# Kernel optimization log

Hardware: AMD Instinct MI355X
Metric: run time of the kernel (lower is better)

## Reference

```python
import jax, jax.numpy as jnp
import numpy as np

N = 50000      # nodes
E = 800000     # edges (before self loops)
IN = 128       # in_channels
H = 8          # heads
C = 32         # hidden_channels per head
HC = H * C     # 256, concat head dim
G = 256        # number of graphs
NEG_SLOPE = 0.2  # PyG GATConv default


def gat_conv(h_in, src, dst, W, att_s, att_d, bias):
    """PyG-style GATConv, concat heads. src/dst include self loops.
    h_in: [N, F_in]; W: [H*C, F_in]; att_s/att_d: [H, C]; bias: [H*C]."""
    h = (h_in @ W.T).reshape(N, H, C)                      # [N,H,C]
    a_s = jnp.sum(h * att_s, axis=-1)                      # [N,H]
    a_d = jnp.sum(h * att_d, axis=-1)                      # [N,H]
    e = jax.nn.leaky_relu(a_s[src] + a_d[dst], NEG_SLOPE)  # [E',H]
    # segment softmax over incoming edges of each dst node
    m = jax.ops.segment_max(e, dst, num_segments=N)        # [N,H]
    p = jnp.exp(e - m[dst])                                # [E',H]
    denom = jax.ops.segment_sum(p, dst, num_segments=N)    # [N,H]
    alpha = p / denom[dst]                                 # [E',H]
    msg = alpha[:, :, None] * h[src]                       # [E',H,C]
    out = jax.ops.segment_sum(msg, dst, num_segments=N)    # [N,H,C]
    return out.reshape(N, HC) + bias


def setup_inputs() -> dict:
    key = jax.random.key(0)
    ks = jax.random.split(key, 20)
    s = 0.1
    inp = {
        "x": jax.random.normal(ks[0], (N, IN), jnp.float32),
        "edge_index": jax.random.randint(ks[1], (2, E), 0, N, dtype=jnp.int64),
        "batch": jnp.sort(jax.random.randint(ks[2], (N,), 0, G, dtype=jnp.int64)),
        # layer 1: IN -> H*C
        "W1": jax.random.normal(ks[3], (HC, IN), jnp.float32) * s,
        "as1": jax.random.normal(ks[4], (H, C), jnp.float32) * s,
        "ad1": jax.random.normal(ks[5], (H, C), jnp.float32) * s,
        "b1": jnp.zeros((HC,), jnp.float32),
        # layer 2: H*C -> H*C
        "W2": jax.random.normal(ks[6], (HC, HC), jnp.float32) * s,
        "as2": jax.random.normal(ks[7], (H, C), jnp.float32) * s,
        "ad2": jax.random.normal(ks[8], (H, C), jnp.float32) * s,
        "b2": jnp.zeros((HC,), jnp.float32),
        # layer 3: H*C -> H*C
        "W3": jax.random.normal(ks[9], (HC, HC), jnp.float32) * s,
        "as3": jax.random.normal(ks[10], (H, C), jnp.float32) * s,
        "ad3": jax.random.normal(ks[11], (H, C), jnp.float32) * s,
        "b3": jnp.zeros((HC,), jnp.float32),
        # final linear H*C -> 1
        "Wf": jax.random.normal(ks[12], (1, HC), jnp.float32) * s,
        "bf": jnp.zeros((1,), jnp.float32),
    }
    return inp


def reference(x, edge_index, batch, W1, as1, ad1, b1, W2, as2, ad2, b2,
              W3, as3, ad3, b3, Wf, bf):
    # add self loops once (PyG GATConv default add_self_loops=True)
    loop = jnp.arange(N, dtype=edge_index.dtype)
    src = jnp.concatenate([edge_index[0], loop])
    dst = jnp.concatenate([edge_index[1], loop])

    h = jax.nn.relu(gat_conv(x, src, dst, W1, as1, ad1, b1))
    # dropout p=0.01, eval mode -> identity
    h = jax.nn.relu(gat_conv(h, src, dst, W2, as2, ad2, b2))
    h = gat_conv(h, src, dst, W3, as3, ad3, b3)

    # global mean pool per graph
    sums = jax.ops.segment_sum(h, batch, num_segments=G)          # [G,HC]
    cnt = jax.ops.segment_sum(jnp.ones((N, 1), h.dtype), batch, num_segments=G)
    pooled = sums / jnp.maximum(cnt, 1.0)                         # [G,HC]
    return pooled @ Wf.T + bf                                     # [G,1]
```

## Files before the change

kernel.cpp:

```cpp
#include <hip/hip_runtime.h>

#define N_NODES 50000
#define E_EDGES 800000
#define E_EXT   850000
#define IN_CH   128
#define HC      256
#define NHEAD   8
#define CH      32
#define NGRAPH  256
#define SCAN_CHUNK 1024
#define N_CHUNKS ((N_NODES + SCAN_CHUNK - 1) / SCAN_CHUNK)

typedef __bf16 bf16x8 __attribute__((ext_vector_type(8)));
typedef float  f32x4  __attribute__((ext_vector_type(4)));

__device__ inline ushort f2bf(float f) {
    union { float f; unsigned u; } v; v.f = f;
    unsigned u = v.u;
    unsigned r = u + 0x7FFFu + ((u >> 16) & 1u);
    return (ushort)(r >> 16);
}
__device__ inline float bflo(unsigned u) {
    union { unsigned u; float f; } v; v.u = u << 16; return v.f;
}
__device__ inline float bfhi(unsigned u) {
    union { unsigned u; float f; } v; v.u = u & 0xFFFF0000u; return v.f;
}

#define W1_N4 (HC * IN_CH / 4)
#define W23_N4 (HC * HC / 4)
#define CVT_N4 (W1_N4 + 2 * W23_N4)
#define COMP_N (32 * HC)
__global__ __launch_bounds__(256) void cvt_weights_kernel(
    const float* __restrict__ W1, const float* __restrict__ W2,
    const float* __restrict__ W3,
    ushort* __restrict__ W1b, ushort* __restrict__ W2b, ushort* __restrict__ W3b,
    const float* __restrict__ as3, const float* __restrict__ ad3,
    const float* __restrict__ b3, const float* __restrict__ Wf,
    float* __restrict__ bw, ushort* __restrict__ Vb)
{
    int i = blockIdx.x * blockDim.x + threadIdx.x;
    if (blockIdx.x == 0 && threadIdx.x < NHEAD) {
        float s = 0.f;
        for (int c = 0; c < CH; c++)
            s += b3[threadIdx.x * CH + c] * Wf[threadIdx.x * CH + c];
        bw[threadIdx.x] = s;
    }
    if (i < CVT_N4) {
        const float* src; ushort* dst; int k;
        if (i < W1_N4) { src = W1; dst = W1b; k = i; }
        else if (i < W1_N4 + W23_N4) { src = W2; dst = W2b; k = i - W1_N4; }
        else { src = W3; dst = W3b; k = i - W1_N4 - W23_N4; }
        float4 v = *(const float4*)(src + (size_t)k * 4);
        ushort4 o;
        o.x = f2bf(v.x); o.y = f2bf(v.y); o.z = f2bf(v.z); o.w = f2bf(v.w);
        *(ushort4*)(dst + (size_t)k * 4) = o;
        return;
    }
    int c2 = i - CVT_N4;
    if (c2 >= COMP_N) return;
    int j = c2 >> 8, k = c2 & 255;
    float v = 0.f;
    if (j < 24) {
        int h = j & 7;
        const float* aw = (j < 8) ? as3 : (j < 16 ? Wf : ad3);
        for (int c = 0; c < CH; c++)
            v += aw[h * CH + c] * W3[(size_t)(h * CH + c) * HC + k];
    }
    Vb[j * HC + k] = f2bf(v);
}

__global__ __launch_bounds__(256) void mfma_gemm_kernel(
    const ushort* __restrict__ Xb, const float* __restrict__ Xf,
    const ushort* __restrict__ Wb,
    ushort* __restrict__ Hb, int M, int F,
    const float* __restrict__ att_s, const float* __restrict__ att_d,
    float* __restrict__ as_out, float* __restrict__ ad_out)
{
    __shared__ ushort As[128][40];
    __shared__ ushort Bs[128][40];
    const int tid  = threadIdx.x;
    const int lane = tid & 63;
    const int wave = tid >> 6;
    const int wr = (wave >> 1) * 64;
    const int wc = (wave & 1) * 64;
    const int bm = blockIdx.x * 128;
    const int bn = blockIdx.y * 128;
    const int lrow = tid >> 2;
    const int lseg = (tid & 3) * 8;
    const int fr = lane & 15;
    const int fk = (lane >> 4) * 8;

    f32x4 zero = {0.f, 0.f, 0.f, 0.f};
    f32x4 acc[4][4];
    #pragma unroll
    for (int i = 0; i < 4; i++)
        #pragma unroll
        for (int j = 0; j < 4; j++) acc[i][j] = zero;

    for (int k0 = 0; k0 < F; k0 += 32) {
        #pragma unroll
        for (int rr = 0; rr < 2; rr++) {
            int row = lrow + rr * 64;
            int arow = bm + row;
            bf16x8 av = {};
            if (Xf) {
                if (arow < M) {
                    float4 lo = *(const float4*)(Xf + (size_t)arow * F + k0 + lseg);
                    float4 hi = *(const float4*)(Xf + (size_t)arow * F + k0 + lseg + 4);
                    ushort t[8] = { f2bf(lo.x), f2bf(lo.y), f2bf(lo.z), f2bf(lo.w),
                                    f2bf(hi.x), f2bf(hi.y), f2bf(hi.z), f2bf(hi.w) };
                    av = *(const bf16x8*)t;
                }
            } else {
                if (arow < M) av = *(const bf16x8*)(Xb + (size_t)arow * F + k0 + lseg);
            }
            *(bf16x8*)(&As[row][lseg]) = av;
            bf16x8 bv = *(const bf16x8*)(Wb + (size_t)(bn + row) * F + k0 + lseg);
            *(bf16x8*)(&Bs[row][lseg]) = bv;
        }
        __syncthreads();
        bf16x8 a[4], b[4];
        #pragma unroll
        for (int i = 0; i < 4; i++) {
            a[i] = *(const bf16x8*)(&As[wr + i * 16 + fr][fk]);
            b[i] = *(const bf16x8*)(&Bs[wc + i * 16 + fr][fk]);
        }
        #pragma unroll
        for (int i = 0; i < 4; i++)
            #pragma unroll
            for (int j = 0; j < 4; j++)
                acc[i][j] = __builtin_amdgcn_mfma_f32_16x16x32_bf16(
                    a[i], b[j], acc[i][j], 0, 0, 0);
        __syncthreads();
    }

    const int rb = (lane >> 4) * 4;
    const int h0 = (bn >> 5) + (wc >> 5);

    const float wsa0 = att_s[h0 * CH + fr],        wsa1 = att_s[h0 * CH + 16 + fr];
    const float wda0 = att_d[h0 * CH + fr],        wda1 = att_d[h0 * CH + 16 + fr];
    const float wsb0 = att_s[(h0 + 1) * CH + fr],  wsb1 = att_s[(h0 + 1) * CH + 16 + fr];
    const float wdb0 = att_d[(h0 + 1) * CH + fr],  wdb1 = att_d[(h0 + 1) * CH + 16 + fr];

    #pragma unroll
    for (int i = 0; i < 4; i++) {
        #pragma unroll
        for (int r = 0; r < 4; r++) {
            int m = bm + wr + i * 16 + rb + r;
            if (m < M) {
                #pragma unroll
                for (int j = 0; j < 4; j++)
                    Hb[(size_t)m * HC + bn + wc + j * 16 + fr] = f2bf(acc[i][j][r]);
            }
            float psa = acc[i][0][r] * wsa0 + acc[i][1][r] * wsa1;
            float pda = acc[i][0][r] * wda0 + acc[i][1][r] * wda1;
            float psb = acc[i][2][r] * wsb0 + acc[i][3][r] * wsb1;
            float pdb = acc[i][2][r] * wdb0 + acc[i][3][r] * wdb1;
            #pragma unroll
            for (int off = 1; off < 16; off <<= 1) {
                psa += __shfl_xor(psa, off);
                pda += __shfl_xor(pda, off);
                psb += __shfl_xor(psb, off);
                pdb += __shfl_xor(pdb, off);
            }
            if (fr == 0 && m < M) {
                as_out[m * NHEAD + h0]     = psa;
                as_out[m * NHEAD + h0 + 1] = psb;
                ad_out[m * NHEAD + h0]     = pda;
                ad_out[m * NHEAD + h0 + 1] = pdb;
            }
        }
    }
}

__global__ __launch_bounds__(256) void gemm3_kernel(
    const ushort* __restrict__ Xb, const ushort* __restrict__ Vb, int M,
    float2* __restrict__ q_out, float* __restrict__ ad_out)
{
    __shared__ ushort As[128][40];
    __shared__ ushort Bs[32][40];
    const int tid  = threadIdx.x;
    const int lane = tid & 63;
    const int wave = tid >> 6;
    const int bm = blockIdx.x * 128;
    const int lrow = tid >> 2;
    const int lseg = (tid & 3) * 8;
    const int fr = lane & 15;
    const int fk = (lane >> 4) * 8;

    f32x4 zero = {0.f, 0.f, 0.f, 0.f};
    f32x4 acc[2][2];
    #pragma unroll
    for (int i = 0; i < 2; i++)
        #pragma unroll
        for (int j = 0; j < 2; j++) acc[i][j] = zero;

    for (int k0 = 0; k0 < HC; k0 += 32) {
        #pragma unroll
        for (int rr = 0; rr < 2; rr++) {
            int row = lrow + rr * 64;
            int arow = bm + row;
            bf16x8 av = {};
            if (arow < M) av = *(const bf16x8*)(Xb + (size_t)arow * HC + k0 + lseg);
            *(bf16x8*)(&As[row][lseg]) = av;
        }
        if (tid < 128) {
            int brow = tid >> 2;
            bf16x8 bv = *(const bf16x8*)(Vb + (size_t)brow * HC + k0 + lseg);
            *(bf16x8*)(&Bs[brow][lseg]) = bv;
        }
        __syncthreads();
        bf16x8 a[2], b[2];
        #pragma unroll
        for (int i = 0; i < 2; i++) {
            a[i] = *(const bf16x8*)(&As[wave * 32 + i * 16 + fr][fk]);
            b[i] = *(const bf16x8*)(&Bs[i * 16 + fr][fk]);
        }
        #pragma unroll
        for (int i = 0; i < 2; i++)
            #pragma unroll
            for (int j = 0; j < 2; j++)
                acc[i][j] = __builtin_amdgcn_mfma_f32_16x16x32_bf16(
                    a[i], b[j], acc[i][j], 0, 0, 0);
        __syncthreads();
    }

    const int rb = (lane >> 4) * 4;
    #pragma unroll
    for (int i = 0; i < 2; i++) {
        #pragma unroll
        for (int r = 0; r < 4; r++) {
            int m = bm + wave * 32 + i * 16 + rb + r;
            if (m >= M) continue;
            #pragma unroll
            for (int j = 0; j < 2; j++) {
                int jj = j * 16 + fr;
                float v = acc[i][j][r];
                if (jj < 8)       ((float*)q_out)[(size_t)(m * NHEAD + jj) * 2]     = v;
                else if (jj < 16) ((float*)q_out)[(size_t)(m * NHEAD + jj - 8) * 2 + 1] = v;
                else if (jj < 24) ad_out[m * NHEAD + jj - 16] = v;
            }
        }
    }
}

__global__ __launch_bounds__(256) void hist_kernel(
    const int* __restrict__ ei, int* __restrict__ deg)
{
    int eid = blockIdx.x * blockDim.x + threadIdx.x;
    if (eid >= E_EXT) return;
    int d = (eid < E_EDGES) ? ei[E_EDGES + eid] : (eid - E_EDGES);
    atomicAdd(&deg[d], 1);
}

__global__ void scan1_kernel(const int* __restrict__ deg,
                             int* __restrict__ row_ptr, int* __restrict__ csum)
{
    __shared__ int buf[SCAN_CHUNK];
    int t = threadIdx.x;
    int base = blockIdx.x * SCAN_CHUNK;
    int v = (base + t < N_NODES) ? deg[base + t] : 0;
    buf[t] = v;
    __syncthreads();
    for (int off = 1; off < SCAN_CHUNK; off <<= 1) {
        int x = buf[t];
        int y = (t >= off) ? buf[t - off] : 0;
        __syncthreads();
        buf[t] = x + y;
        __syncthreads();
    }
    if (base + t < N_NODES) row_ptr[base + t] = buf[t] - v;
    if (t == SCAN_CHUNK - 1) csum[blockIdx.x] = buf[t];
}

__global__ void scan2_kernel(int* __restrict__ csum)
{
    __shared__ int buf[64];
    int t = threadIdx.x;
    int v = (t < N_CHUNKS) ? csum[t] : 0;
    buf[t] = v;
    __syncthreads();
    for (int off = 1; off < 64; off <<= 1) {
        int x = buf[t];
        int y = (t >= off) ? buf[t - off] : 0;
        __syncthreads();
        buf[t] = x + y;
        __syncthreads();
    }
    if (t < N_CHUNKS) csum[t] = buf[t] - v;
}

__global__ void scan3_kernel(int* __restrict__ row_ptr, const int* __restrict__ csum)
{
    int i = blockIdx.x * blockDim.x + threadIdx.x;
    if (i < N_NODES) row_ptr[i] += csum[i / SCAN_CHUNK];
    if (i == 0) row_ptr[N_NODES] = E_EXT;
}

__global__ __launch_bounds__(256) void scatter_kernel(
    const int* __restrict__ ei, const int* __restrict__ row_ptr,
    int* __restrict__ cur, int* __restrict__ esrc)
{
    int eid = blockIdx.x * blockDim.x + threadIdx.x;
    if (eid >= E_EXT) return;
    int s, d;
    if (eid < E_EDGES) { s = ei[eid]; d = ei[E_EDGES + eid]; }
    else { s = eid - E_EDGES; d = s; }
    int pos = row_ptr[d] + atomicAdd(&cur[d], 1);
    esrc[pos] = s;
}

__global__ __launch_bounds__(256) void gather_kernel(
    const int* __restrict__ row_ptr, const int* __restrict__ esrc,
    const ushort* __restrict__ hb,
    const float* __restrict__ a_s, const float* __restrict__ a_d,
    const float* __restrict__ bias,
    ushort* __restrict__ out_b)
{
    int wv = (blockIdx.x * blockDim.x + threadIdx.x) >> 6;
    int lane = threadIdx.x & 63;
    int half = lane >> 5;
    int lloc = lane & 31;
    int n = wv * 2 + half;
    if (n >= N_NODES) return;
    const int hh = lloc >> 2;
    const int shbase = half << 5;
    const float adv = a_d[n * NHEAD + hh];
    const int beg = row_ptr[n], end = row_ptr[n + 1];

    float a0=0.f,a1=0.f,a2=0.f,a3=0.f,a4=0.f,a5=0.f,a6=0.f,a7=0.f,den=0.f;

    for (int base = beg; base < end; base += 32) {
        int cnt = min(32, end - base);
        int sv = (base + lloc < end) ? esrc[base + lloc] : 0;
        int j = 0;
        for (; j + 4 <= cnt; j += 4) {
            int s0 = __shfl(sv, shbase + j);
            int s1 = __shfl(sv, shbase + j + 1);
            int s2 = __shfl(sv, shbase + j + 2);
            int s3 = __shfl(sv, shbase + j + 3);
            float e0 = a_s[s0 * NHEAD + hh];
            float e1 = a_s[s1 * NHEAD + hh];
            float e2 = a_s[s2 * NHEAD + hh];
            float e3 = a_s[s3 * NHEAD + hh];
            uint4 u0 = *(const uint4*)(hb + (size_t)s0 * HC + lloc * 8);
            uint4 u1 = *(const uint4*)(hb + (size_t)s1 * HC + lloc * 8);
            uint4 u2 = *(const uint4*)(hb + (size_t)s2 * HC + lloc * 8);
            uint4 u3 = *(const uint4*)(hb + (size_t)s3 * HC + lloc * 8);
            e0 += adv; e0 = (e0 > 0.f) ? e0 : 0.2f * e0; float w0 = __expf(e0);
            e1 += adv; e1 = (e1 > 0.f) ? e1 : 0.2f * e1; float w1 = __expf(e1);
            e2 += adv; e2 = (e2 > 0.f) ? e2 : 0.2f * e2; float w2 = __expf(e2);
            e3 += adv; e3 = (e3 > 0.f) ? e3 : 0.2f * e3; float w3 = __expf(e3);
            den += (w0 + w1) + (w2 + w3);
            a0 = fmaf(w0, bflo(u0.x), a0); a1 = fmaf(w0, bfhi(u0.x), a1);
            a2 = fmaf(w0, bflo(u0.y), a2); a3 = fmaf(w0, bfhi(u0.y), a3);
            a4 = fmaf(w0, bflo(u0.z), a4); a5 = fmaf(w0, bfhi(u0.z), a5);
            a6 = fmaf(w0, bflo(u0.w), a6); a7 = fmaf(w0, bfhi(u0.w), a7);
            a0 = fmaf(w1, bflo(u1.x), a0); a1 = fmaf(w1, bfhi(u1.x), a1);
            a2 = fmaf(w1, bflo(u1.y), a2); a3 = fmaf(w1, bfhi(u1.y), a3);
            a4 = fmaf(w1, bflo(u1.z), a4); a5 = fmaf(w1, bfhi(u1.z), a5);
            a6 = fmaf(w1, bflo(u1.w), a6); a7 = fmaf(w1, bfhi(u1.w), a7);
            a0 = fmaf(w2, bflo(u2.x), a0); a1 = fmaf(w2, bfhi(u2.x), a1);
            a2 = fmaf(w2, bflo(u2.y), a2); a3 = fmaf(w2, bfhi(u2.y), a3);
            a4 = fmaf(w2, bflo(u2.z), a4); a5 = fmaf(w2, bfhi(u2.z), a5);
            a6 = fmaf(w2, bflo(u2.w), a6); a7 = fmaf(w2, bfhi(u2.w), a7);
            a0 = fmaf(w3, bflo(u3.x), a0); a1 = fmaf(w3, bfhi(u3.x), a1);
            a2 = fmaf(w3, bflo(u3.y), a2); a3 = fmaf(w3, bfhi(u3.y), a3);
            a4 = fmaf(w3, bflo(u3.z), a4); a5 = fmaf(w3, bfhi(u3.z), a5);
            a6 = fmaf(w3, bflo(u3.w), a6); a7 = fmaf(w3, bfhi(u3.w), a7);
        }
        for (; j < cnt; j++) {
            int s = __shfl(sv, shbase + j);
            float e = a_s[s * NHEAD + hh] + adv;
            e = (e > 0.f) ? e : 0.2f * e;
            float w = __expf(e);
            den += w;
            uint4 u = *(const uint4*)(hb + (size_t)s * HC + lloc * 8);
            a0 = fmaf(w, bflo(u.x), a0); a1 = fmaf(w, bfhi(u.x), a1);
            a2 = fmaf(w, bflo(u.y), a2); a3 = fmaf(w, bfhi(u.y), a3);
            a4 = fmaf(w, bflo(u.z), a4); a5 = fmaf(w, bfhi(u.z), a5);
            a6 = fmaf(w, bflo(u.w), a6); a7 = fmaf(w, bfhi(u.w), a7);
        }
    }
    float inv = 1.f / den;
    float4 ba = *(const float4*)(bias + lloc * 8);
    float4 bb = *(const float4*)(bias + lloc * 8 + 4);
    float o0 = fmaf(a0, inv, ba.x), o1 = fmaf(a1, inv, ba.y);
    float o2 = fmaf(a2, inv, ba.z), o3 = fmaf(a3, inv, ba.w);
    float o4 = fmaf(a4, inv, bb.x), o5 = fmaf(a5, inv, bb.y);
    float o6 = fmaf(a6, inv, bb.z), o7 = fmaf(a7, inv, bb.w);
    o0 = fmaxf(o0, 0.f); o1 = fmaxf(o1, 0.f); o2 = fmaxf(o2, 0.f); o3 = fmaxf(o3, 0.f);
    o4 = fmaxf(o4, 0.f); o5 = fmaxf(o5, 0.f); o6 = fmaxf(o6, 0.f); o7 = fmaxf(o7, 0.f);
    uint4 ob;
    ob.x = (unsigned)f2bf(o0) | ((unsigned)f2bf(o1) << 16);
    ob.y = (unsigned)f2bf(o2) | ((unsigned)f2bf(o3) << 16);
    ob.z = (unsigned)f2bf(o4) | ((unsigned)f2bf(o5) << 16);
    ob.w = (unsigned)f2bf(o6) | ((unsigned)f2bf(o7) << 16);
    *(uint4*)(out_b + (size_t)n * HC + lloc * 8) = ob;
}

__global__ __launch_bounds__(256) void light_gather_kernel(
    const int* __restrict__ row_ptr, const int* __restrict__ esrc,
    const float2* __restrict__ q, const float* __restrict__ a_d,
    const float* __restrict__ bw, float* __restrict__ ndot)
{
    int idx = blockIdx.x * blockDim.x + threadIdx.x;
    if (idx >= N_NODES * NHEAD) return;
    int n = idx >> 3, hh = idx & 7;
    const float adv = a_d[idx];
    const int beg = row_ptr[n], end = row_ptr[n + 1];
    float acc = 0.f, den = 0.f;
    int e = beg;
    for (; e + 4 <= end; e += 4) {
        int s0 = esrc[e], s1 = esrc[e + 1], s2 = esrc[e + 2], s3 = esrc[e + 3];
        float2 q0 = q[s0 * NHEAD + hh];
        float2 q1 = q[s1 * NHEAD + hh];
        float2 q2 = q[s2 * NHEAD + hh];
        float2 q3 = q[s3 * NHEAD + hh];
        float t0 = q0.x + adv; t0 = (t0 > 0.f) ? t0 : 0.2f * t0; float w0 = __expf(t0);
        float t1 = q1.x + adv; t1 = (t1 > 0.f) ? t1 : 0.2f * t1; float w1 = __expf(t1);
        float t2 = q2.x + adv; t2 = (t2 > 0.f) ? t2 : 0.2f * t2; float w2 = __expf(t2);
        float t3 = q3.x + adv; t3 = (t3 > 0.f) ? t3 : 0.2f * t3; float w3 = __expf(t3);
        den += (w0 + w1) + (w2 + w3);
        acc = fmaf(w0, q0.y, acc); acc = fmaf(w1, q1.y, acc);
        acc = fmaf(w2, q2.y, acc); acc = fmaf(w3, q3.y, acc);
    }
    for (; e < end; e++) {
        int s = esrc[e];
        float2 qv = q[s * NHEAD + hh];
        float t = qv.x + adv; t = (t > 0.f) ? t : 0.2f * t;
        float w = __expf(t);
        den += w;
        acc = fmaf(w, qv.y, acc);
    }
    float p = acc / den + bw[hh];
    #pragma unroll
    for (int off = 4; off > 0; off >>= 1) p += __shfl_xor(p, off);
    if (hh == 0) ndot[n] = p;
}

__global__ __launch_bounds__(256) void pool2_kernel(
    const float* __restrict__ ndot, const int* __restrict__ batch,
    const float* __restrict__ bf, float* __restrict__ outp)
{
    __shared__ float red[256];
    int g = blockIdx.x, t = threadIdx.x;
    int lo = 0, hi = N_NODES;
    while (lo < hi) { int mid = (lo + hi) >> 1; if (batch[mid] < g) lo = mid + 1; else hi = mid; }
    int start = lo;
    lo = 0; hi = N_NODES;
    while (lo < hi) { int mid = (lo + hi) >> 1; if (batch[mid] < g + 1) lo = mid + 1; else hi = mid; }
    int end = lo;
    float s = 0.f;
    for (int i = start + t; i < end; i += 256) s += ndot[i];
    red[t] = s;
    __syncthreads();
    for (int k = 128; k > 0; k >>= 1) {
        if (t < k) red[t] += red[t + k];
        __syncthreads();
    }
    if (t == 0) outp[g] = red[0] / fmaxf((float)(end - start), 1.f) + bf[0];
}

extern "C" void kernel_launch(void* const* d_in, const int* in_sizes, int n_in,
                              void* d_out, int out_size, void* d_ws, size_t ws_size,
                              hipStream_t stream)
{
    const float* x    = (const float*)d_in[0];
    const int*   ei   = (const int*)d_in[1];
    const int*   batch= (const int*)d_in[2];
    const float* W1   = (const float*)d_in[3];
    const float* as1  = (const float*)d_in[4];
    const float* ad1  = (const float*)d_in[5];
    const float* b1   = (const float*)d_in[6];
    const float* W2   = (const float*)d_in[7];
    const float* as2  = (const float*)d_in[8];
    const float* ad2  = (const float*)d_in[9];
    const float* b2   = (const float*)d_in[10];
    const float* W3   = (const float*)d_in[11];
    const float* as3  = (const float*)d_in[12];
    const float* ad3  = (const float*)d_in[13];
    const float* b3   = (const float*)d_in[14];
    const float* Wf   = (const float*)d_in[15];
    const float* bf   = (const float*)d_in[16];
    float* out = (float*)d_out;

    char* ws = (char*)d_ws;
    size_t off = 0;
    auto allocb = [&](size_t bytes) {
        void* p = ws + off;
        off += (bytes + 255) & ~(size_t)255;
        return p;
    };
    ushort* bufA    = (ushort*)allocb((size_t)N_NODES * HC * 2);
    ushort* bufB    = (ushort*)allocb((size_t)N_NODES * HC * 2);
    ushort* W1b     = (ushort*)allocb((size_t)HC * IN_CH * 2);
    ushort* W2b     = (ushort*)allocb((size_t)HC * HC * 2);
    ushort* W3b     = (ushort*)allocb((size_t)HC * HC * 2);
    ushort* Vb      = (ushort*)allocb((size_t)32 * HC * 2);
    float*  as_buf  = (float*) allocb((size_t)N_NODES * NHEAD * 4);
    float*  ad_buf  = (float*) allocb((size_t)N_NODES * NHEAD * 4);
    float2* q_buf   = (float2*)allocb((size_t)N_NODES * NHEAD * 8);
    float*  bw_buf  = (float*) allocb(NHEAD * 4);
    int*    deg     = (int*)   allocb(N_NODES * 4);
    int*    cur     = (int*)   allocb(N_NODES * 4);
    int*    row_ptr = (int*)   allocb((N_NODES + 1) * 4);
    int*    csum    = (int*)   allocb(64 * 4);
    int*    esrc    = (int*)   allocb(E_EXT * 4);
    float*  ndot    = (float*) allocb(N_NODES * 4);
    (void)ws_size; (void)in_sizes; (void)n_in; (void)out_size;

    cvt_weights_kernel<<<(CVT_N4 + COMP_N + 255) / 256, 256, 0, stream>>>(
        W1, W2, W3, W1b, W2b, W3b, as3, ad3, b3, Wf, bw_buf, Vb);

    const size_t deg_pad = ((size_t)N_NODES * 4 + 255) & ~(size_t)255;
    hipMemsetAsync(deg, 0, deg_pad + (size_t)N_NODES * 4, stream);
    hist_kernel<<<(E_EXT + 255) / 256, 256, 0, stream>>>(ei, deg);
    scan1_kernel<<<N_CHUNKS, SCAN_CHUNK, 0, stream>>>(deg, row_ptr, csum);
    scan2_kernel<<<1, 64, 0, stream>>>(csum);
    scan3_kernel<<<(N_NODES + 255) / 256, 256, 0, stream>>>(row_ptr, csum);
    scatter_kernel<<<(E_EXT + 255) / 256, 256, 0, stream>>>(ei, row_ptr, cur, esrc);

    dim3 ggrid((N_NODES + 127) / 128, HC / 128);
    const int gather_blocks = (((N_NODES + 1) / 2) * 64 + 255) / 256;

    mfma_gemm_kernel<<<ggrid, 256, 0, stream>>>(
        nullptr, x, W1b, bufB, N_NODES, IN_CH, as1, ad1, as_buf, ad_buf);
    gather_kernel<<<gather_blocks, 256, 0, stream>>>(
        row_ptr, esrc, bufB, as_buf, ad_buf, b1, bufA);
    mfma_gemm_kernel<<<ggrid, 256, 0, stream>>>(
        bufA, nullptr, W2b, bufB, N_NODES, HC, as2, ad2, as_buf, ad_buf);
    gather_kernel<<<gather_blocks, 256, 0, stream>>>(
        row_ptr, esrc, bufB, as_buf, ad_buf, b2, bufA);
    gemm3_kernel<<<(N_NODES + 127) / 128, 256, 0, stream>>>(
        bufA, Vb, N_NODES, q_buf, ad_buf);
    light_gather_kernel<<<(N_NODES * NHEAD + 255) / 256, 256, 0, stream>>>(
        row_ptr, esrc, q_buf, ad_buf, bw_buf, ndot);

    pool2_kernel<<<NGRAPH, 256, 0, stream>>>(ndot, batch, bf, out);
}
```

Measured before the change: 319.1 us.

## Precompute attention projections via folded weights and merge prep kernels

```diff
diff --git a/kernel.cpp b/kernel.cpp
--- a/kernel.cpp
+++ b/kernel.cpp
@@ -30,14 +30,21 @@
 #define W1_N4 (HC * IN_CH / 4)
 #define W23_N4 (HC * HC / 4)
 #define CVT_N4 (W1_N4 + 2 * W23_N4)
-#define COMP_N (32 * HC)
-__global__ __launch_bounds__(256) void cvt_weights_kernel(
+#define V1_N  (32 * IN_CH)
+#define V23_N (32 * HC)
+#define COMP_TOT (V1_N + 2 * V23_N)
+#define PREP_TOT (CVT_N4 + COMP_TOT + E_EXT)
+__global__ __launch_bounds__(256) void prep_kernel(
     const float* __restrict__ W1, const float* __restrict__ W2,
     const float* __restrict__ W3,
     ushort* __restrict__ W1b, ushort* __restrict__ W2b, ushort* __restrict__ W3b,
+    const float* __restrict__ as1, const float* __restrict__ ad1,
+    const float* __restrict__ as2, const float* __restrict__ ad2,
     const float* __restrict__ as3, const float* __restrict__ ad3,
     const float* __restrict__ b3, const float* __restrict__ Wf,
-    float* __restrict__ bw, ushort* __restrict__ Vb)
+    float* __restrict__ bw,
+    ushort* __restrict__ Vb1, ushort* __restrict__ Vb2, ushort* __restrict__ Vb3,
+    const int* __restrict__ ei, int* __restrict__ deg)
 {
     int i = blockIdx.x * blockDim.x + threadIdx.x;
     if (blockIdx.x == 0 && threadIdx.x < NHEAD) {
@@ -58,24 +65,40 @@
         return;
     }
     int c2 = i - CVT_N4;
-    if (c2 >= COMP_N) return;
-    int j = c2 >> 8, k = c2 & 255;
-    float v = 0.f;
-    if (j < 24) {
-        int h = j & 7;
-        const float* aw = (j < 8) ? as3 : (j < 16 ? Wf : ad3);
-        for (int c = 0; c < CH; c++)
-            v += aw[h * CH + c] * W3[(size_t)(h * CH + c) * HC + k];
-    }
-    Vb[j * HC + k] = f2bf(v);
+    if (c2 < COMP_TOT) {
+        const float* Wsrc; const float* aw; ushort* dst; int F_, j, k;
+        if (c2 < V1_N) {
+            F_ = IN_CH; j = c2 >> 7; k = c2 & 127; Wsrc = W1; dst = Vb1;
+            aw = (j < 8) ? as1 : ad1;
+        } else if (c2 < V1_N + V23_N) {
+            c2 -= V1_N;
+            F_ = HC; j = c2 >> 8; k = c2 & 255; Wsrc = W2; dst = Vb2;
+            aw = (j < 8) ? as2 : ad2;
+        } else {
+            c2 -= V1_N + V23_N;
+            F_ = HC; j = c2 >> 8; k = c2 & 255; Wsrc = W3; dst = Vb3;
+            aw = (j < 8) ? as3 : (j < 16 ? Wf : ad3);
+        }
+        float v = 0.f;
+        if (j < ((dst == Vb3) ? 24 : 16)) {
+            int h = j & 7;
+            for (int c = 0; c < CH; c++)
+                v += aw[h * CH + c] * Wsrc[(size_t)(h * CH + c) * F_ + k];
+        }
+        dst[j * F_ + k] = f2bf(v);
+        return;
+    }
+    int e = i - CVT_N4 - COMP_TOT;
+    if (e < E_EXT) {
+        int d = (e < E_EDGES) ? ei[E_EDGES + e] : (e - E_EDGES);
+        atomicAdd(&deg[d], 1);
+    }
 }
 
 __global__ __launch_bounds__(256) void mfma_gemm_kernel(
     const ushort* __restrict__ Xb, const float* __restrict__ Xf,
     const ushort* __restrict__ Wb,
-    ushort* __restrict__ Hb, int M, int F,
-    const float* __restrict__ att_s, const float* __restrict__ att_d,
-    float* __restrict__ as_out, float* __restrict__ ad_out)
+    ushort* __restrict__ Hb, int M, int F)
 {
     __shared__ ushort As[128][40];
     __shared__ ushort Bs[128][40];
@@ -134,15 +157,7 @@
                     a[i], b[j], acc[i][j], 0, 0, 0);
         __syncthreads();
     }
-
     const int rb = (lane >> 4) * 4;
-    const int h0 = (bn >> 5) + (wc >> 5);
-
-    const float wsa0 = att_s[h0 * CH + fr],        wsa1 = att_s[h0 * CH + 16 + fr];
-    const float wda0 = att_d[h0 * CH + fr],        wda1 = att_d[h0 * CH + 16 + fr];
-    const float wsb0 = att_s[(h0 + 1) * CH + fr],  wsb1 = att_s[(h0 + 1) * CH + 16 + fr];
-    const float wdb0 = att_d[(h0 + 1) * CH + fr],  wdb1 = att_d[(h0 + 1) * CH + 16 + fr];
-
     #pragma unroll
     for (int i = 0; i < 4; i++) {
         #pragma unroll
@@ -153,30 +168,15 @@
                 for (int j = 0; j < 4; j++)
                     Hb[(size_t)m * HC + bn + wc + j * 16 + fr] = f2bf(acc[i][j][r]);
             }
-            float psa = acc[i][0][r] * wsa0 + acc[i][1][r] * wsa1;
-            float pda = acc[i][0][r] * wda0 + acc[i][1][r] * wda1;
-            float psb = acc[i][2][r] * wsb0 + acc[i][3][r] * wsb1;
-            float pdb = acc[i][2][r] * wdb0 + acc[i][3][r] * wdb1;
-            #pragma unroll
-            for (int off = 1; off < 16; off <<= 1) {
-                psa += __shfl_xor(psa, off);
-                pda += __shfl_xor(pda, off);
-                psb += __shfl_xor(psb, off);
-                pdb += __shfl_xor(pdb, off);
-            }
-            if (fr == 0 && m < M) {
-                as_out[m * NHEAD + h0]     = psa;
-                as_out[m * NHEAD + h0 + 1] = psb;
-                ad_out[m * NHEAD + h0]     = pda;
-                ad_out[m * NHEAD + h0 + 1] = pdb;
-            }
-        }
-    }
-}
-
-__global__ __launch_bounds__(256) void gemm3_kernel(
-    const ushort* __restrict__ Xb, const ushort* __restrict__ Vb, int M,
-    float2* __restrict__ q_out, float* __restrict__ ad_out)
+        }
+    }
+}
+
+__global__ __launch_bounds__(256) void thin_gemm_kernel(
+    const ushort* __restrict__ Xb, const float* __restrict__ Xf,
+    const ushort* __restrict__ Vb, int M, int F, int mode,
+    float* __restrict__ as_out, float* __restrict__ ad_out,
+    float2* __restrict__ q_out)
 {
     __shared__ ushort As[128][40];
     __shared__ ushort Bs[32][40];
@@ -196,33 +196,43 @@
         #pragma unroll
         for (int j = 0; j < 2; j++) acc[i][j] = zero;
 
-    for (int k0 = 0; k0 < HC; k0 += 32) {
+    for (int k0 = 0; k0 < F; k0 += 32) {
         #pragma unroll
         for (int rr = 0; rr < 2; rr++) {
             int row = lrow + rr * 64;
             int arow = bm + row;
             bf16x8 av = {};
-            if (arow < M) av = *(const bf16x8*)(Xb + (size_t)arow * HC + k0 + lseg);
+            if (Xf) {
+                if (arow < M) {
+                    float4 lo = *(const float4*)(Xf + (size_t)arow * F + k0 + lseg);
+                    float4 hi = *(const float4*)(Xf + (size_t)arow * F + k0 + lseg + 4);
+                    ushort t[8] = { f2bf(lo.x), f2bf(lo.y), f2bf(lo.z), f2bf(lo.w),
+                                    f2bf(hi.x), f2bf(hi.y), f2bf(hi.z), f2bf(hi.w) };
+                    av = *(const bf16x8*)t;
+                }
+            } else {
+                if (arow < M) av = *(const bf16x8*)(Xb + (size_t)arow * F + k0 + lseg);
+            }
             *(bf16x8*)(&As[row][lseg]) = av;
         }
         if (tid < 128) {
             int brow = tid >> 2;
-            bf16x8 bv = *(const bf16x8*)(Vb + (size_t)brow * HC + k0 + lseg);
+            bf16x8 bv = *(const bf16x8*)(Vb + (size_t)brow * F + k0 + lseg);
             *(bf16x8*)(&Bs[brow][lseg]) = bv;
         }
         __syncthreads();
-        bf16x8 a[2], b[2];
-        #pragma unroll
-        for (int i = 0; i < 2; i++) {
+        bf16x8 a[2];
+        #pragma unroll
+        for (int i = 0; i < 2; i++)
             a[i] = *(const bf16x8*)(&As[wave * 32 + i * 16 + fr][fk]);
-            b[i] = *(const bf16x8*)(&Bs[i * 16 + fr][fk]);
-        }
-        #pragma unroll
-        for (int i = 0; i < 2; i++)
-            #pragma unroll
-            for (int j = 0; j < 2; j++)
-                acc[i][j] = __builtin_amdgcn_mfma_f32_16x16x32_bf16(
-                    a[i], b[j], acc[i][j], 0, 0, 0);
+        bf16x8 b0 = *(const bf16x8*)(&Bs[fr][fk]);
+        acc[0][0] = __builtin_amdgcn_mfma_f32_16x16x32_bf16(a[0], b0, acc[0][0], 0, 0, 0);
+        acc[1][0] = __builtin_amdgcn_mfma_f32_16x16x32_bf16(a[1], b0, acc[1][0], 0, 0, 0);
+        if (mode) {
+            bf16x8 b1 = *(const bf16x8*)(&Bs[16 + fr][fk]);
+            acc[0][1] = __builtin_amdgcn_mfma_f32_16x16x32_bf16(a[0], b1, acc[0][1], 0, 0, 0);
+            acc[1][1] = __builtin_amdgcn_mfma_f32_16x16x32_bf16(a[1], b1, acc[1][1], 0, 0, 0);
+        }
         __syncthreads();
     }
 
@@ -237,21 +247,17 @@
             for (int j = 0; j < 2; j++) {
                 int jj = j * 16 + fr;
                 float v = acc[i][j][r];
-                if (jj < 8)       ((float*)q_out)[(size_t)(m * NHEAD + jj) * 2]     = v;
-                else if (jj < 16) ((float*)q_out)[(size_t)(m * NHEAD + jj - 8) * 2 + 1] = v;
-                else if (jj < 24) ad_out[m * NHEAD + jj - 16] = v;
+                if (mode == 0) {
+                    if (jj < 8)       as_out[m * NHEAD + jj] = v;
+                    else if (jj < 16) ad_out[m * NHEAD + jj - 8] = v;
+                } else {
+                    if (jj < 8)       ((float*)q_out)[(size_t)(m * NHEAD + jj) * 2] = v;
+                    else if (jj < 16) ((float*)q_out)[(size_t)(m * NHEAD + jj - 8) * 2 + 1] = v;
+                    else if (jj < 24) ad_out[m * NHEAD + jj - 16] = v;
+                }
             }
         }
     }
-}
-
-__global__ __launch_bounds__(256) void hist_kernel(
-    const int* __restrict__ ei, int* __restrict__ deg)
-{
-    int eid = blockIdx.x * blockDim.x + threadIdx.x;
-    if (eid >= E_EXT) return;
-    int d = (eid < E_EDGES) ? ei[E_EDGES + eid] : (eid - E_EDGES);
-    atomicAdd(&deg[d], 1);
 }
 
 __global__ void scan1_kernel(const int* __restrict__ deg,
@@ -274,27 +280,25 @@
     if (t == SCAN_CHUNK - 1) csum[blockIdx.x] = buf[t];
 }
 
-__global__ void scan2_kernel(int* __restrict__ csum)
-{
-    __shared__ int buf[64];
+__global__ __launch_bounds__(256) void scan23_kernel(
+    int* __restrict__ row_ptr, const int* __restrict__ csum)
+{
+    __shared__ int pref[64];
     int t = threadIdx.x;
-    int v = (t < N_CHUNKS) ? csum[t] : 0;
-    buf[t] = v;
+    int i = blockIdx.x * blockDim.x + t;
+    if (t < 64) pref[t] = (t < N_CHUNKS) ? csum[t] : 0;
     __syncthreads();
     for (int off = 1; off < 64; off <<= 1) {
-        int x = buf[t];
-        int y = (t >= off) ? buf[t - off] : 0;
-        __syncthreads();
-        buf[t] = x + y;
-        __syncthreads();
-    }
-    if (t < N_CHUNKS) csum[t] = buf[t] - v;
-}
-
-__global__ void scan3_kernel(int* __restrict__ row_ptr, const int* __restrict__ csum)
-{
-    int i = blockIdx.x * blockDim.x + threadIdx.x;
-    if (i < N_NODES) row_ptr[i] += csum[i / SCAN_CHUNK];
+        int x = 0, y = 0;
+        if (t < 64) { x = pref[t]; y = (t >= off) ? pref[t - off] : 0; }
+        __syncthreads();
+        if (t < 64) pref[t] = x + y;
+        __syncthreads();
+    }
+    if (i < N_NODES) {
+        int ch = i / SCAN_CHUNK;
+        row_ptr[i] += (ch > 0) ? pref[ch - 1] : 0;
+    }
     if (i == 0) row_ptr[N_NODES] = E_EXT;
 }
 
@@ -498,7 +502,9 @@
     ushort* W1b     = (ushort*)allocb((size_t)HC * IN_CH * 2);
     ushort* W2b     = (ushort*)allocb((size_t)HC * HC * 2);
     ushort* W3b     = (ushort*)allocb((size_t)HC * HC * 2);
-    ushort* Vb      = (ushort*)allocb((size_t)32 * HC * 2);
+    ushort* Vb1     = (ushort*)allocb((size_t)32 * IN_CH * 2);
+    ushort* Vb2     = (ushort*)allocb((size_t)32 * HC * 2);
+    ushort* Vb3     = (ushort*)allocb((size_t)32 * HC * 2);
     float*  as_buf  = (float*) allocb((size_t)N_NODES * NHEAD * 4);
     float*  ad_buf  = (float*) allocb((size_t)N_NODES * NHEAD * 4);
     float2* q_buf   = (float2*)allocb((size_t)N_NODES * NHEAD * 8);
@@ -511,30 +517,36 @@
     float*  ndot    = (float*) allocb(N_NODES * 4);
     (void)ws_size; (void)in_sizes; (void)n_in; (void)out_size;
 
-    cvt_weights_kernel<<<(CVT_N4 + COMP_N + 255) / 256, 256, 0, stream>>>(
-        W1, W2, W3, W1b, W2b, W3b, as3, ad3, b3, Wf, bw_buf, Vb);
-
     const size_t deg_pad = ((size_t)N_NODES * 4 + 255) & ~(size_t)255;
     hipMemsetAsync(deg, 0, deg_pad + (size_t)N_NODES * 4, stream);
-    hist_kernel<<<(E_EXT + 255) / 256, 256, 0, stream>>>(ei, deg);
+
+    prep_kernel<<<(PREP_TOT + 255) / 256, 256, 0, stream>>>(
+        W1, W2, W3, W1b, W2b, W3b,
+        as1, ad1, as2, ad2, as3, ad3, b3, Wf, bw_buf,
+        Vb1, Vb2, Vb3, ei, deg);
+
     scan1_kernel<<<N_CHUNKS, SCAN_CHUNK, 0, stream>>>(deg, row_ptr, csum);
-    scan2_kernel<<<1, 64, 0, stream>>>(csum);
-    scan3_kernel<<<(N_NODES + 255) / 256, 256, 0, stream>>>(row_ptr, csum);
+    scan23_kernel<<<(N_NODES + 255) / 256, 256, 0, stream>>>(row_ptr, csum);
     scatter_kernel<<<(E_EXT + 255) / 256, 256, 0, stream>>>(ei, row_ptr, cur, esrc);
 
     dim3 ggrid((N_NODES + 127) / 128, HC / 128);
     const int gather_blocks = (((N_NODES + 1) / 2) * 64 + 255) / 256;
+    const int thin_blocks = (N_NODES + 127) / 128;
 
     mfma_gemm_kernel<<<ggrid, 256, 0, stream>>>(
-        nullptr, x, W1b, bufB, N_NODES, IN_CH, as1, ad1, as_buf, ad_buf);
+        nullptr, x, W1b, bufB, N_NODES, IN_CH);
+    thin_gemm_kernel<<<thin_blocks, 256, 0, stream>>>(
+        nullptr, x, Vb1, N_NODES, IN_CH, 0, as_buf, ad_buf, nullptr);
     gather_kernel<<<gather_blocks, 256, 0, stream>>>(
         row_ptr, esrc, bufB, as_buf, ad_buf, b1, bufA);
     mfma_gemm_kernel<<<ggrid, 256, 0, stream>>>(
-        bufA, nullptr, W2b, bufB, N_NODES, HC, as2, ad2, as_buf, ad_buf);
+        bufA, nullptr, W2b, bufB, N_NODES, HC);
+    thin_gemm_kernel<<<thin_blocks, 256, 0, stream>>>(
+        bufA, nullptr, Vb2, N_NODES, HC, 0, as_buf, ad_buf, nullptr);
     gather_kernel<<<gather_blocks, 256, 0, stream>>>(
         row_ptr, esrc, bufB, as_buf, ad_buf, b2, bufA);
-    gemm3_kernel<<<(N_NODES + 127) / 128, 256, 0, stream>>>(
-        bufA, Vb, N_NODES, q_buf, ad_buf);
+    thin_gemm_kernel<<<thin_blocks, 256, 0, stream>>>(
+        bufA, nullptr, Vb3, N_NODES, HC, 1, nullptr, ad_buf, q_buf);
     light_gather_kernel<<<(N_NODES * NHEAD + 255) / 256, 256, 0, stream>>>(
         row_ptr, esrc, q_buf, ad_buf, bw_buf, ndot);
 
```

Measured after the change: 325.5 us. +2.0%, slower.
